# Kernel tuning notes

Hardware: AMD Instinct MI355X
Metric: run time of the kernel (lower is better)

The kernel has to match this reference:

```python
import jax, jax.numpy as jnp
import numpy as np

EMBED_DIM = 1024
N_HEADS = 16
HEAD_DIM = EMBED_DIM // N_HEADS
MAX_REL_POS = 2  # hardcoded in the torch module


def _rel_index(length_q, length_k):
    # final_mat[i, j] = clip(i - j, -p, p) + p  with i over k-range, j over q-range
    rq = jnp.arange(length_q)[None, :]
    rk = jnp.arange(length_k)[:, None]
    dist = jnp.clip(rk - rq, -MAX_REL_POS, MAX_REL_POS) + MAX_REL_POS
    return dist  # (len_k, len_q) int; square when len_q == len_k


def setup_inputs() -> dict:
    key = jax.random.key(0)
    ks = jax.random.split(key, 16)
    B, S, E, H, D = 4, 1024, EMBED_DIM, N_HEADS, HEAD_DIM
    xavier = lambda k, shape: jax.random.uniform(
        k, shape, jnp.float32, -1.0, 1.0) * np.sqrt(6.0 / (shape[0] + shape[1]))
    return {
        "query": jax.random.normal(ks[0], (B, S, E), jnp.float32),
        "key": jax.random.normal(ks[1], (B, S, E), jnp.float32),
        "value": jax.random.normal(ks[2], (B, S, E), jnp.float32),
        "Wq": xavier(ks[3], (E, E)), "bq": jnp.zeros((E,), jnp.float32),
        "Wk": xavier(ks[4], (E, E)), "bk": jnp.zeros((E,), jnp.float32),
        "Wv": xavier(ks[5], (E, E)), "bv": jnp.zeros((E,), jnp.float32),
        "Wo": xavier(ks[6], (E, E)), "bo": jnp.zeros((E,), jnp.float32),
        "rpk_table": xavier(ks[7], (2 * MAX_REL_POS + 1, D)),
        "rpv_table": xavier(ks[8], (2 * MAX_REL_POS + 1, D)),
    }


def reference(query, key, value, Wq, bq, Wk, bk, Wv, bv, Wo, bo, rpk_table, rpv_table):
    B, S, E = query.shape
    H, D = N_HEADS, HEAD_DIM
    q = query @ Wq.T + bq
    _k = key @ Wk.T + bk      # computed but unused (faithful to source bug)
    v = value @ Wv.T + bv

    qh = q.reshape(B, S, H, D).transpose(0, 2, 1, 3)   # b h s d
    vh = v.reshape(B, S, H, D).transpose(0, 2, 1, 3)

    # NOTE: source uses query for both sides of the dot product
    dots = jnp.einsum('bhqd,bhkd->bhqk', qh, qh)

    idx = _rel_index(S, S)                              # (S, S)
    rpk = rpk_table[idx]                                # (S, S, D)
    rp_dots = jnp.einsum('bhqd,qkd->bhqk', qh, rpk)

    scale = jnp.sqrt(jnp.asarray(D, q.dtype))
    attn = jax.nn.softmax((dots + rp_dots) / scale, axis=-1)

    weight1 = jnp.einsum('bhqk,bhkd->bhqd', attn, vh)
    rpv = rpv_table[idx]                                # (S, S, D)
    weight2 = jnp.einsum('bhqk,qkd->bhqd', attn, rpv)

    out = (weight1 + weight2).transpose(0, 2, 1, 3).reshape(B, S, E)
    return out @ Wo.T + bo
```

## Files before the change

### kernel.cpp

```cpp
#include <hip/hip_runtime.h>


typedef _Float16 v8h __attribute__((ext_vector_type(8)));
typedef _Float16 v4h __attribute__((ext_vector_type(4)));
typedef float    v4f __attribute__((ext_vector_type(4)));

#define MFMA_F16(A_, B_, C_) __builtin_amdgcn_mfma_f32_16x16x32_f16(A_, B_, C_, 0, 0, 0)

__device__ __forceinline__ void async_copy16(const void* g, void* l) {
    __builtin_amdgcn_global_load_lds(
        (const __attribute__((address_space(1))) void*)g,
        (__attribute__((address_space(3))) void*)l, 16, 0, 0);
}

__global__ __launch_bounds__(256) void cvt5_kernel(
    const float* __restrict__ s0, const float* __restrict__ s1,
    const float* __restrict__ s2, const float* __restrict__ s3,
    const float* __restrict__ s4,
    _Float16* __restrict__ d0, _Float16* __restrict__ d1,
    _Float16* __restrict__ d2, _Float16* __restrict__ d3,
    _Float16* __restrict__ d4,
    int n0, int n1, int n2, int n3, int n4)
{
    const float* s; _Float16* d; int n;
    switch (blockIdx.y) {
        case 0:  s = s0; d = d0; n = n0; break;
        case 1:  s = s1; d = d1; n = n1; break;
        case 2:  s = s2; d = d2; n = n2; break;
        case 3:  s = s3; d = d3; n = n3; break;
        default: s = s4; d = d4; n = n4; break;
    }
    int i = (blockIdx.x * 256 + threadIdx.x) * 4;
    if (i >= n) return;
    float4 f = *(const float4*)(s + i);
    v4h o = { (_Float16)f.x, (_Float16)f.y, (_Float16)f.z, (_Float16)f.w };
    *(v4h*)(d + i) = o;
}

__device__ __forceinline__ void gemm_core(const _Float16* __restrict__ A,
                                          const _Float16* __restrict__ W,
                                          const float* __restrict__ bias,
                                          int mode, void* __restrict__ outp)
{
    __shared__ __align__(16) _Float16 As[128 * 64];
    __shared__ __align__(16) _Float16 Bs[128 * 64];

    const int tid  = threadIdx.x;
    const int wave = tid >> 6, lane = tid & 63;
    const int quad = lane >> 4, n16 = lane & 15;
    const int wm = wave >> 1, wn = wave & 1;
    const int row0 = blockIdx.y * 128, col0 = blockIdx.x * 128;
    const int rL = lane >> 3, c8 = lane & 7;
    const int lcs = c8 ^ rL;

    v4f acc[4][4] = {};

    for (int kb = 0; kb < 1024; kb += 64) {
        __syncthreads();
        #pragma unroll
        for (int p = 0; p < 4; p++) {
            int c = wave * 4 + p;
            int row = c * 8 + rL;
            async_copy16(A + (size_t)(row0 + row) * 1024 + kb + lcs * 8, &As[c * 512]);
            async_copy16(W + (size_t)(col0 + row) * 1024 + kb + lcs * 8, &Bs[c * 512]);
        }
        __syncthreads();
        #pragma unroll
        for (int ks = 0; ks < 64; ks += 32) {
            const int pc = ((ks >> 3) + quad) ^ (n16 & 7);
            v8h af[4], bf[4];
            #pragma unroll
            for (int i = 0; i < 4; i++)
                af[i] = *(const v8h*)(&As[(wm * 64 + i * 16 + n16) * 64 + pc * 8]);
            #pragma unroll
            for (int j = 0; j < 4; j++)
                bf[j] = *(const v8h*)(&Bs[(wn * 64 + j * 16 + n16) * 64 + pc * 8]);
            #pragma unroll
            for (int i = 0; i < 4; i++)
                #pragma unroll
                for (int j = 0; j < 4; j++)
                    acc[i][j] = MFMA_F16(af[i], bf[j], acc[i][j]);
        }
    }

    #pragma unroll
    for (int i = 0; i < 4; i++)
        #pragma unroll
        for (int j = 0; j < 4; j++)
            #pragma unroll
            for (int r = 0; r < 4; r++) {
                int row = row0 + wm * 64 + i * 16 + quad * 4 + r;
                int col = col0 + wn * 64 + j * 16 + n16;
                float v = acc[i][j][r] + bias[col];
                if (mode == 0) {
                    int b = row >> 10, s = row & 1023, h = col >> 6, d = col & 63;
                    ((_Float16*)outp)[(((size_t)(b * 16 + h)) * 1024 + s) * 64 + d] = (_Float16)v;
                } else if (mode == 1) {
                    int b = row >> 10, s = row & 1023, h = col >> 6, d = col & 63;
                    ((_Float16*)outp)[(((size_t)(b * 16 + h)) * 64 + d) * 1024 + s] = (_Float16)v;
                } else {
                    ((float*)outp)[(size_t)row * 1024 + col] = v;
                }
            }
}

__global__ __launch_bounds__(256) void gemm_qv_kernel(
    const _Float16* __restrict__ Aq, const _Float16* __restrict__ Av,
    const _Float16* __restrict__ Wq, const _Float16* __restrict__ Wv,
    const float* __restrict__ bq, const float* __restrict__ bv,
    _Float16* __restrict__ q_out, _Float16* __restrict__ v_out)
{
    int z = blockIdx.z;
    gemm_core(z ? Av : Aq, z ? Wv : Wq, z ? bv : bq, z ? 1 : 0,
              z ? (void*)v_out : (void*)q_out);
}

__global__ __launch_bounds__(256) void gemm_o_kernel(
    const _Float16* __restrict__ A, const _Float16* __restrict__ W,
    const float* __restrict__ bias, float* __restrict__ outp)
{
    gemm_core(A, W, bias, 2, (void*)outp);
}

__global__ __launch_bounds__(256) void attn_kernel(
    const _Float16* __restrict__ qb,
    const _Float16* __restrict__ vt,
    const float* __restrict__ rpk, const float* __restrict__ rpv,
    _Float16* __restrict__ attn_o)
{
    const int bh = blockIdx.y;
    const int q0 = blockIdx.x * 64;
    const int tid = threadIdx.x;
    const int wave = tid >> 6, lane = tid & 63;
    const int quad = lane >> 4, n16 = lane & 15;
    const int qw = q0 + wave * 16;
    const _Float16* Qh = qb + (size_t)bh * 1024 * 64;
    const _Float16* Vh = vt + (size_t)bh * 64 * 1024;

    __shared__ __align__(16) _Float16 Ks[64 * 64];
    __shared__ __align__(16) _Float16 Vs[64 * 64];
    __shared__ __align__(16) _Float16 Ps[4][16 * 64];
    __shared__ float rqs[4][16][6];

    {
        int m = lane >> 2, seg = lane & 3;
        const _Float16* qrow = Qh + (size_t)(qw + m) * 64 + seg * 16;
        v8h qa = *(const v8h*)(qrow);
        v8h qc = *(const v8h*)(qrow + 8);
        float qd[16];
        #pragma unroll
        for (int x = 0; x < 8; x++) { qd[x] = (float)qa[x]; qd[8 + x] = (float)qc[x]; }
        float qq = 0.f;
        #pragma unroll
        for (int x = 0; x < 16; x++) qq += qd[x] * qd[x];
        qq += __shfl_xor(qq, 1);
        qq += __shfl_xor(qq, 2);
        #pragma unroll
        for (int t = 0; t < 5; t++) {
            float s = 0.f;
            #pragma unroll
            for (int x = 0; x < 16; x++) s += qd[x] * rpk[t * 64 + seg * 16 + x];
            s += __shfl_xor(s, 1);
            s += __shfl_xor(s, 2);
            if (seg == 0) rqs[wave][m][t] = (s - qq) * 0.125f;
        }
    }
    __syncthreads();

    float rc[4][5];
    #pragma unroll
    for (int r = 0; r < 4; r++)
        #pragma unroll
        for (int t = 0; t < 5; t++)
            rc[r][t] = rqs[wave][quad * 4 + r][t];

    v8h aq0 = *(const v8h*)(Qh + (size_t)(qw + n16) * 64 + quad * 8);
    v8h aq1 = *(const v8h*)(Qh + (size_t)(qw + n16) * 64 + 32 + quad * 8);

    float lrow[4] = {}, blo[4] = {}, bm1[4] = {}, bc0[4] = {}, bp1[4] = {};
    v4f O[4] = {};

    const int rL = lane >> 3, c8 = lane & 7;
    const int lcs = c8 ^ rL;
    const int pphys0 = quad ^ (n16 & 7);
    const int pphys1 = (quad + 4) ^ (n16 & 7);

    for (int kb = 0; kb < 1024; kb += 64) {
        __syncthreads();
        #pragma unroll
        for (int p = 0; p < 2; p++) {
            int c = wave * 2 + p;
            int row = c * 8 + rL;
            async_copy16(Qh + (size_t)(kb + row) * 64 + lcs * 8, &Ks[c * 512]);
            async_copy16(Vh + (size_t)row * 1024 + kb + lcs * 8, &Vs[c * 512]);
        }
        __syncthreads();

        float pp4[4][4];
        #pragma unroll
        for (int t = 0; t < 4; t++) {
            v8h bk0 = *(const v8h*)(&Ks[(t * 16 + n16) * 64 + pphys0 * 8]);
            v8h bk1 = *(const v8h*)(&Ks[(t * 16 + n16) * 64 + pphys1 * 8]);
            v4f s = {0.f, 0.f, 0.f, 0.f};
            s = MFMA_F16(aq0, bk0, s);
            s = MFMA_F16(aq1, bk1, s);
            const int dq = qw - (kb + t * 16);
            if (dq >= 32) {
                #pragma unroll
                for (int r = 0; r < 4; r++) {
                    float p = __expf(fmaf(s[r], 0.125f, rc[r][4]));
                    pp4[t][r] = p; lrow[r] += p; blo[r] += p;
                }
            } else if (dq <= -32) {
                #pragma unroll
                for (int r = 0; r < 4; r++) {
                    float p = __expf(fmaf(s[r], 0.125f, rc[r][0]));
                    pp4[t][r] = p; lrow[r] += p;
                }
            } else {
                #pragma unroll
                for (int r = 0; r < 4; r++) {
                    int diff = dq + quad * 4 + r - n16;
                    float rv = diff >= 2  ? rc[r][4]
                             : diff == 1  ? rc[r][3]
                             : diff == 0  ? rc[r][2]
                             : diff == -1 ? rc[r][1]
                                          : rc[r][0];
                    float p = __expf(fmaf(s[r], 0.125f, rv));
                    pp4[t][r] = p; lrow[r] += p;
                    if (diff >= 2)       blo[r] += p;
                    else if (diff == 1)  bm1[r] += p;
                    else if (diff == 0)  bc0[r] += p;
                    else if (diff == -1) bp1[r] += p;
                }
            }
        }

        #pragma unroll
        for (int t = 0; t < 4; t++)
            #pragma unroll
            for (int r = 0; r < 4; r++) {
                int row = quad * 4 + r, pcol = t * 16 + n16;
                int pc = (pcol >> 3) ^ (row & 7);
                Ps[wave][row * 64 + pc * 8 + (pcol & 7)] = (_Float16)pp4[t][r];
            }

        v8h pf0 = *(const v8h*)(&Ps[wave][n16 * 64 + pphys0 * 8]);
        v8h pf1 = *(const v8h*)(&Ps[wave][n16 * 64 + pphys1 * 8]);
        #pragma unroll
        for (int dt = 0; dt < 4; dt++) {
            v8h v0 = *(const v8h*)(&Vs[(dt * 16 + n16) * 64 + pphys0 * 8]);
            v8h v1 = *(const v8h*)(&Vs[(dt * 16 + n16) * 64 + pphys1 * 8]);
            O[dt] = MFMA_F16(pf0, v0, O[dt]);
            O[dt] = MFMA_F16(pf1, v1, O[dt]);
        }
    }

    #pragma unroll
    for (int r = 0; r < 4; r++) {
        float l = lrow[r], lo = blo[r], a1 = bm1[r], a0 = bc0[r], ap = bp1[r];
        #pragma unroll
        for (int off = 1; off < 16; off <<= 1) {
            l  += __shfl_xor(l,  off);
            lo += __shfl_xor(lo, off);
            a1 += __shfl_xor(a1, off);
            a0 += __shfl_xor(a0, off);
            ap += __shfl_xor(ap, off);
        }
        float hi  = l - lo - a1 - a0 - ap;
        float inv = 1.0f / l;
        int qg = qw + quad * 4 + r;
        int brow = (bh >> 4) * 1024 + qg;
        int hcol = (bh & 15) * 64;
        #pragma unroll
        for (int dt = 0; dt < 4; dt++) {
            int d = dt * 16 + n16;
            float w2 = lo * rpv[4 * 64 + d] + a1 * rpv[3 * 64 + d] + a0 * rpv[2 * 64 + d]
                     + ap * rpv[1 * 64 + d] + hi * rpv[0 * 64 + d];
            float val = (O[dt][r] + w2) * inv;
            attn_o[(size_t)brow * 1024 + hcol + d] = (_Float16)val;
        }
    }
}

extern "C" void kernel_launch(void* const* d_in, const int* in_sizes, int n_in,
                              void* d_out, int out_size, void* d_ws, size_t ws_size,
                              hipStream_t stream)
{
    const float* query = (const float*)d_in[0];
    const float* value = (const float*)d_in[2];
    const float* Wq = (const float*)d_in[3];
    const float* bq = (const float*)d_in[4];
    const float* Wv = (const float*)d_in[7];
    const float* bv = (const float*)d_in[8];
    const float* Wo = (const float*)d_in[9];
    const float* bo = (const float*)d_in[10];
    const float* rpk = (const float*)d_in[11];
    const float* rpv = (const float*)d_in[12];
    float* out = (float*)d_out;

    char* ws = (char*)d_ws;
    const size_t MB = 1024 * 1024;
    _Float16* q_bhsd = (_Float16*)(ws);
    _Float16* v_t    = (_Float16*)(ws + 8 * MB);
    _Float16* q16    = (_Float16*)(ws + 16 * MB);
    _Float16* attn_o = (_Float16*)(ws + 16 * MB);
    _Float16* v16    = (_Float16*)(ws + 24 * MB);
    _Float16* wq16   = (_Float16*)(ws + 32 * MB);
    _Float16* wv16   = (_Float16*)(ws + 34 * MB);
    _Float16* wo16   = (_Float16*)(ws + 36 * MB);

    cvt5_kernel<<<dim3(4096, 5), 256, 0, stream>>>(
        query, value, Wq, Wv, Wo, q16, v16, wq16, wv16, wo16,
        4096 * 1024, 4096 * 1024, 1024 * 1024, 1024 * 1024, 1024 * 1024);

    gemm_qv_kernel<<<dim3(8, 32, 2), 256, 0, stream>>>(
        q16, v16, wq16, wv16, bq, bv, q_bhsd, v_t);

    attn_kernel<<<dim3(16, 64), 256, 0, stream>>>(q_bhsd, v_t, rpk, rpv, attn_o);

    gemm_o_kernel<<<dim3(8, 32), 256, 0, stream>>>(attn_o, wo16, bo, out);
}
```

Measured before the change: 232.1 us.

## Stage GEMM epilogues through LDS, shrink output GEMM tile, transpose attention MFMA

The GEMM epilogues now write results into LDS with a swizzle and then issue 16-byte vectorized global stores, replacing scattered 2-byte and 4-byte writes. This matters most for the transposed V layout and the head-split Q layout. The output-projection GEMM moves to 64-row tiles, doubling its grid to 512 blocks for better CU occupancy. The attention kernel swaps MFMA operand order so each lane owns one query row, which removes the cross-lane row reductions, packs P writes as v4h, and stores output as vectors. The attention grid is also flattened to 1-D with heads interleaved, which may change L2 locality.

```diff
diff --git a/kernel.cpp b/kernel.cpp
--- a/kernel.cpp
+++ b/kernel.cpp
@@ -37,19 +37,24 @@
     *(v4h*)(d + i) = o;
 }
 
+template<int TM>
 __device__ __forceinline__ void gemm_core(const _Float16* __restrict__ A,
                                           const _Float16* __restrict__ W,
                                           const float* __restrict__ bias,
                                           int mode, void* __restrict__ outp)
 {
-    __shared__ __align__(16) _Float16 As[128 * 64];
-    __shared__ __align__(16) _Float16 Bs[128 * 64];
+    __shared__ __align__(16) _Float16 smem[2 * 128 * 64];
+    _Float16* As = smem;
+    _Float16* Bs = smem + 128 * 64;
 
     const int tid  = threadIdx.x;
     const int wave = tid >> 6, lane = tid & 63;
     const int quad = lane >> 4, n16 = lane & 15;
-    const int wm = wave >> 1, wn = wave & 1;
-    const int row0 = blockIdx.y * 128, col0 = blockIdx.x * 128;
+    const int wm = (TM == 128) ? (wave >> 1) : 0;
+    const int wn = (TM == 128) ? (wave & 1) : wave;
+    const int WCOLS = (TM == 128) ? 64 : 32;
+    const int NJ = WCOLS / 16;
+    const int row0 = blockIdx.y * TM, col0 = blockIdx.x * 128;
     const int rL = lane >> 3, c8 = lane & 7;
     const int lcs = c8 ^ rL;
 
@@ -58,11 +63,16 @@
     for (int kb = 0; kb < 1024; kb += 64) {
         __syncthreads();
         #pragma unroll
+        for (int p = 0; p < TM / 32; p++) {
+            int rg = wave * (TM / 32) + p;
+            int row = rg * 8 + rL;
+            async_copy16(A + (size_t)(row0 + row) * 1024 + kb + lcs * 8, &As[rg * 512]);
+        }
+        #pragma unroll
         for (int p = 0; p < 4; p++) {
-            int c = wave * 4 + p;
-            int row = c * 8 + rL;
-            async_copy16(A + (size_t)(row0 + row) * 1024 + kb + lcs * 8, &As[c * 512]);
-            async_copy16(W + (size_t)(col0 + row) * 1024 + kb + lcs * 8, &Bs[c * 512]);
+            int rg = wave * 4 + p;
+            int row = rg * 8 + rL;
+            async_copy16(W + (size_t)(col0 + row) * 1024 + kb + lcs * 8, &Bs[rg * 512]);
         }
         __syncthreads();
         #pragma unroll
@@ -73,35 +83,84 @@
             for (int i = 0; i < 4; i++)
                 af[i] = *(const v8h*)(&As[(wm * 64 + i * 16 + n16) * 64 + pc * 8]);
             #pragma unroll
+            for (int j = 0; j < NJ; j++)
+                bf[j] = *(const v8h*)(&Bs[(wn * WCOLS + j * 16 + n16) * 64 + pc * 8]);
+            #pragma unroll
+            for (int i = 0; i < 4; i++)
+                #pragma unroll
+                for (int j = 0; j < NJ; j++)
+                    acc[i][j] = MFMA_F16(af[i], bf[j], acc[i][j]);
+        }
+    }
+
+    __syncthreads();
+    char* scb = (char*)smem + wave * 8192;
+
+    const int b     = (row0 + wm * 64) >> 10;
+    const int srow0 = (row0 + wm * 64) & 1023;
+
+    if (mode == 0) {
+        _Float16* sc = (_Float16*)scb;
+        #pragma unroll
+        for (int i = 0; i < 4; i++)
+            #pragma unroll
             for (int j = 0; j < 4; j++)
-                bf[j] = *(const v8h*)(&Bs[(wn * 64 + j * 16 + n16) * 64 + pc * 8]);
-            #pragma unroll
-            for (int i = 0; i < 4; i++)
-                #pragma unroll
-                for (int j = 0; j < 4; j++)
-                    acc[i][j] = MFMA_F16(af[i], bf[j], acc[i][j]);
-        }
-    }
-
-    #pragma unroll
-    for (int i = 0; i < 4; i++)
-        #pragma unroll
-        for (int j = 0; j < 4; j++)
-            #pragma unroll
-            for (int r = 0; r < 4; r++) {
-                int row = row0 + wm * 64 + i * 16 + quad * 4 + r;
-                int col = col0 + wn * 64 + j * 16 + n16;
-                float v = acc[i][j][r] + bias[col];
-                if (mode == 0) {
-                    int b = row >> 10, s = row & 1023, h = col >> 6, d = col & 63;
-                    ((_Float16*)outp)[(((size_t)(b * 16 + h)) * 1024 + s) * 64 + d] = (_Float16)v;
-                } else if (mode == 1) {
-                    int b = row >> 10, s = row & 1023, h = col >> 6, d = col & 63;
-                    ((_Float16*)outp)[(((size_t)(b * 16 + h)) * 64 + d) * 1024 + s] = (_Float16)v;
-                } else {
-                    ((float*)outp)[(size_t)row * 1024 + col] = v;
-                }
+                #pragma unroll
+                for (int r = 0; r < 4; r++) {
+                    int rowL = i * 16 + quad * 4 + r, colL = j * 16 + n16;
+                    float v = acc[i][j][r] + bias[col0 + wn * 64 + colL];
+                    sc[rowL * 64 + (((colL >> 3) ^ (rowL & 7)) << 3) + (colL & 7)] = (_Float16)v;
+                }
+        int h = (col0 + wn * 64) >> 6;
+        #pragma unroll
+        for (int it = 0; it < 8; it++) {
+            int rowR = it * 8 + (lane >> 3), cR = lane & 7;
+            v8h val = *(const v8h*)(&sc[rowR * 64 + ((cR ^ (rowR & 7)) << 3)]);
+            *(v8h*)((_Float16*)outp +
+                    (((size_t)(b * 16 + h) * 1024 + srow0 + rowR) << 6) + cR * 8) = val;
+        }
+    } else if (mode == 1) {
+        _Float16* sc = (_Float16*)scb;
+        #pragma unroll
+        for (int i = 0; i < 4; i++)
+            #pragma unroll
+            for (int j = 0; j < 4; j++) {
+                int colL = j * 16 + n16;
+                int c16 = i * 2 + (quad >> 1);
+                v4h pk;
+                #pragma unroll
+                for (int r = 0; r < 4; r++)
+                    pk[r] = (_Float16)(acc[i][j][r] + bias[col0 + wn * 64 + colL]);
+                *(v4h*)(&sc[colL * 64 + ((c16 ^ (colL & 7)) << 3) + (quad & 1) * 4]) = pk;
             }
+        #pragma unroll
+        for (int it = 0; it < 8; it++) {
+            int dR = it * 8 + (lane >> 3), scn = lane & 7;
+            v8h val = *(const v8h*)(&sc[dR * 64 + ((scn ^ (dR & 7)) << 3)]);
+            int cg = col0 + wn * 64 + dR;
+            int h = cg >> 6, dl = cg & 63;
+            *(v8h*)((_Float16*)outp +
+                    ((size_t)((b * 16 + h) * 64 + dl) << 10) + srow0 + scn * 8) = val;
+        }
+    } else {
+        float* sc = (float*)scb;
+        #pragma unroll
+        for (int i = 0; i < 4; i++)
+            #pragma unroll
+            for (int j = 0; j < 2; j++)
+                #pragma unroll
+                for (int r = 0; r < 4; r++) {
+                    int rowL = i * 16 + quad * 4 + r, colL = j * 16 + n16;
+                    sc[rowL * 32 + (((colL >> 2) ^ (rowL & 7)) << 2) + (colL & 3)] =
+                        acc[i][j][r] + bias[col0 + wn * 32 + colL];
+                }
+        #pragma unroll
+        for (int it = 0; it < 8; it++) {
+            int rowR = it * 8 + (lane >> 3), cR = lane & 7;
+            v4f val = *(const v4f*)(&sc[rowR * 32 + ((cR ^ (rowR & 7)) << 2)]);
+            *(v4f*)((float*)outp + (size_t)(row0 + rowR) * 1024 + col0 + wn * 32 + cR * 4) = val;
+        }
+    }
 }
 
 __global__ __launch_bounds__(256) void gemm_qv_kernel(
@@ -111,15 +170,15 @@
     _Float16* __restrict__ q_out, _Float16* __restrict__ v_out)
 {
     int z = blockIdx.z;
-    gemm_core(z ? Av : Aq, z ? Wv : Wq, z ? bv : bq, z ? 1 : 0,
-              z ? (void*)v_out : (void*)q_out);
+    gemm_core<128>(z ? Av : Aq, z ? Wv : Wq, z ? bv : bq, z ? 1 : 0,
+                   z ? (void*)v_out : (void*)q_out);
 }
 
 __global__ __launch_bounds__(256) void gemm_o_kernel(
     const _Float16* __restrict__ A, const _Float16* __restrict__ W,
     const float* __restrict__ bias, float* __restrict__ outp)
 {
-    gemm_core(A, W, bias, 2, (void*)outp);
+    gemm_core<64>(A, W, bias, 2, (void*)outp);
 }
 
 __global__ __launch_bounds__(256) void attn_kernel(
@@ -128,8 +187,9 @@
     const float* __restrict__ rpk, const float* __restrict__ rpv,
     _Float16* __restrict__ attn_o)
 {
-    const int bh = blockIdx.y;
-    const int q0 = blockIdx.x * 64;
+    const int blk = blockIdx.x;
+    const int bh = blk & 63;
+    const int q0 = (blk >> 6) * 64;
     const int tid = threadIdx.x;
     const int wave = tid >> 6, lane = tid & 63;
     const int quad = lane >> 4, n16 = lane & 15;
@@ -140,7 +200,7 @@
     __shared__ __align__(16) _Float16 Ks[64 * 64];
     __shared__ __align__(16) _Float16 Vs[64 * 64];
     __shared__ __align__(16) _Float16 Ps[4][16 * 64];
-    __shared__ float rqs[4][16][6];
+    __shared__ float rqs[4][16][5];
 
     {
         int m = lane >> 2, seg = lane & 3;
@@ -167,17 +227,14 @@
     }
     __syncthreads();
 
-    float rc[4][5];
+    float rc[5];
     #pragma unroll
-    for (int r = 0; r < 4; r++)
-        #pragma unroll
-        for (int t = 0; t < 5; t++)
-            rc[r][t] = rqs[wave][quad * 4 + r][t];
+    for (int t = 0; t < 5; t++) rc[t] = rqs[wave][n16][t];
 
     v8h aq0 = *(const v8h*)(Qh + (size_t)(qw + n16) * 64 + quad * 8);
     v8h aq1 = *(const v8h*)(Qh + (size_t)(qw + n16) * 64 + 32 + quad * 8);
 
-    float lrow[4] = {}, blo[4] = {}, bm1[4] = {}, bc0[4] = {}, bp1[4] = {};
+    float bkt[5] = {0.f, 0.f, 0.f, 0.f, 0.f};
     v4f O[4] = {};
 
     const int rL = lane >> 3, c8 = lane & 7;
@@ -196,90 +253,83 @@
         }
         __syncthreads();
 
-        float pp4[4][4];
         #pragma unroll
         for (int t = 0; t < 4; t++) {
-            v8h bk0 = *(const v8h*)(&Ks[(t * 16 + n16) * 64 + pphys0 * 8]);
-            v8h bk1 = *(const v8h*)(&Ks[(t * 16 + n16) * 64 + pphys1 * 8]);
+            v8h ak0 = *(const v8h*)(&Ks[(t * 16 + n16) * 64 + pphys0 * 8]);
+            v8h ak1 = *(const v8h*)(&Ks[(t * 16 + n16) * 64 + pphys1 * 8]);
             v4f s = {0.f, 0.f, 0.f, 0.f};
-            s = MFMA_F16(aq0, bk0, s);
-            s = MFMA_F16(aq1, bk1, s);
-            const int dq = qw - (kb + t * 16);
-            if (dq >= 32) {
-                #pragma unroll
-                for (int r = 0; r < 4; r++) {
-                    float p = __expf(fmaf(s[r], 0.125f, rc[r][4]));
-                    pp4[t][r] = p; lrow[r] += p; blo[r] += p;
-                }
-            } else if (dq <= -32) {
-                #pragma unroll
-                for (int r = 0; r < 4; r++) {
-                    float p = __expf(fmaf(s[r], 0.125f, rc[r][0]));
-                    pp4[t][r] = p; lrow[r] += p;
+            s = MFMA_F16(ak0, aq0, s);
+            s = MFMA_F16(ak1, aq1, s);
+            const int dqt = qw - kb - t * 16;
+            float pv[4];
+            if (dqt >= 32) {
+                #pragma unroll
+                for (int r = 0; r < 4; r++) {
+                    float p = __expf(fmaf(s[r], 0.125f, rc[4]));
+                    pv[r] = p; bkt[4] += p;
+                }
+            } else if (dqt <= -32) {
+                #pragma unroll
+                for (int r = 0; r < 4; r++) {
+                    float p = __expf(fmaf(s[r], 0.125f, rc[0]));
+                    pv[r] = p; bkt[0] += p;
                 }
             } else {
                 #pragma unroll
                 for (int r = 0; r < 4; r++) {
-                    int diff = dq + quad * 4 + r - n16;
-                    float rv = diff >= 2  ? rc[r][4]
-                             : diff == 1  ? rc[r][3]
-                             : diff == 0  ? rc[r][2]
-                             : diff == -1 ? rc[r][1]
-                                          : rc[r][0];
+                    int diff = dqt + n16 - quad * 4 - r;
+                    float rv = diff >= 2  ? rc[4]
+                             : diff == 1  ? rc[3]
+                             : diff == 0  ? rc[2]
+                             : diff == -1 ? rc[1]
+                                          : rc[0];
                     float p = __expf(fmaf(s[r], 0.125f, rv));
-                    pp4[t][r] = p; lrow[r] += p;
-                    if (diff >= 2)       blo[r] += p;
-                    else if (diff == 1)  bm1[r] += p;
-                    else if (diff == 0)  bc0[r] += p;
-                    else if (diff == -1) bp1[r] += p;
+                    pv[r] = p;
+                    bkt[4] += (diff >= 2)  ? p : 0.f;
+                    bkt[3] += (diff == 1)  ? p : 0.f;
+                    bkt[2] += (diff == 0)  ? p : 0.f;
+                    bkt[1] += (diff == -1) ? p : 0.f;
+                    bkt[0] += (diff <= -2) ? p : 0.f;
                 }
             }
-        }
-
-        #pragma unroll
-        for (int t = 0; t < 4; t++)
-            #pragma unroll
-            for (int r = 0; r < 4; r++) {
-                int row = quad * 4 + r, pcol = t * 16 + n16;
-                int pc = (pcol >> 3) ^ (row & 7);
-                Ps[wave][row * 64 + pc * 8 + (pcol & 7)] = (_Float16)pp4[t][r];
-            }
+            v4h pk = { (_Float16)pv[0], (_Float16)pv[1], (_Float16)pv[2], (_Float16)pv[3] };
+            int c16 = t * 2 + (quad >> 1);
+            *(v4h*)(&Ps[wave][n16 * 64 + ((c16 ^ (n16 & 7)) << 3) + (quad & 1) * 4]) = pk;
+        }
 
         v8h pf0 = *(const v8h*)(&Ps[wave][n16 * 64 + pphys0 * 8]);
         v8h pf1 = *(const v8h*)(&Ps[wave][n16 * 64 + pphys1 * 8]);
         #pragma unroll
         for (int dt = 0; dt < 4; dt++) {
-            v8h v0 = *(const v8h*)(&Vs[(dt * 16 + n16) * 64 + pphys0 * 8]);
-            v8h v1 = *(const v8h*)(&Vs[(dt * 16 + n16) * 64 + pphys1 * 8]);
-            O[dt] = MFMA_F16(pf0, v0, O[dt]);
-            O[dt] = MFMA_F16(pf1, v1, O[dt]);
+            v8h av0 = *(const v8h*)(&Vs[(dt * 16 + n16) * 64 + pphys0 * 8]);
+            v8h av1 = *(const v8h*)(&Vs[(dt * 16 + n16) * 64 + pphys1 * 8]);
+            O[dt] = MFMA_F16(av0, pf0, O[dt]);
+            O[dt] = MFMA_F16(av1, pf1, O[dt]);
         }
     }
 
     #pragma unroll
-    for (int r = 0; r < 4; r++) {
-        float l = lrow[r], lo = blo[r], a1 = bm1[r], a0 = bc0[r], ap = bp1[r];
-        #pragma unroll
-        for (int off = 1; off < 16; off <<= 1) {
-            l  += __shfl_xor(l,  off);
-            lo += __shfl_xor(lo, off);
-            a1 += __shfl_xor(a1, off);
-            a0 += __shfl_xor(a0, off);
-            ap += __shfl_xor(ap, off);
-        }
-        float hi  = l - lo - a1 - a0 - ap;
-        float inv = 1.0f / l;
-        int qg = qw + quad * 4 + r;
-        int brow = (bh >> 4) * 1024 + qg;
-        int hcol = (bh & 15) * 64;
-        #pragma unroll
-        for (int dt = 0; dt < 4; dt++) {
-            int d = dt * 16 + n16;
-            float w2 = lo * rpv[4 * 64 + d] + a1 * rpv[3 * 64 + d] + a0 * rpv[2 * 64 + d]
-                     + ap * rpv[1 * 64 + d] + hi * rpv[0 * 64 + d];
-            float val = (O[dt][r] + w2) * inv;
-            attn_o[(size_t)brow * 1024 + hcol + d] = (_Float16)val;
-        }
+    for (int t = 0; t < 5; t++) {
+        bkt[t] += __shfl_xor(bkt[t], 16);
+        bkt[t] += __shfl_xor(bkt[t], 32);
+    }
+    float l = bkt[0] + bkt[1] + bkt[2] + bkt[3] + bkt[4];
+    float inv = 1.0f / l;
+    int q = qw + n16;
+    size_t orow = (size_t)((bh >> 4) * 1024 + q) * 1024 + (bh & 15) * 64;
+    #pragma unroll
+    for (int dt = 0; dt < 4; dt++) {
+        int d0 = dt * 16 + quad * 4;
+        v4h st;
+        #pragma unroll
+        for (int r = 0; r < 4; r++) {
+            int d = d0 + r;
+            float w2 = bkt[4] * rpv[4 * 64 + d] + bkt[3] * rpv[3 * 64 + d]
+                     + bkt[2] * rpv[2 * 64 + d] + bkt[1] * rpv[1 * 64 + d]
+                     + bkt[0] * rpv[0 * 64 + d];
+            st[r] = (_Float16)((O[dt][r] + w2) * inv);
+        }
+        *(v4h*)(attn_o + orow + d0) = st;
     }
 }
 
@@ -317,7 +367,7 @@
     gemm_qv_kernel<<<dim3(8, 32, 2), 256, 0, stream>>>(
         q16, v16, wq16, wv16, bq, bv, q_bhsd, v_t);
 
-    attn_kernel<<<dim3(16, 64), 256, 0, stream>>>(q_bhsd, v_t, rpk, rpv, attn_o);
-
-    gemm_o_kernel<<<dim3(8, 32), 256, 0, stream>>>(attn_o, wo16, bo, out);
-}
+    attn_kernel<<<dim3(1024), 256, 0, stream>>>(q_bhsd, v_t, rpk, rpv, attn_o);
+
+    gemm_o_kernel<<<dim3(8, 64), 256, 0, stream>>>(attn_o, wo16, bo, out);
+}
```

New measurement: 203.4 us. -12.3%, faster.
